# Kernel tuning notes

Hardware: AMD Instinct MI355X
Metric: run time of the kernel (lower is better)

## Reference

```python
import jax, jax.numpy as jnp
import numpy as np

BETA = 1.0
DEPTH = 10
LEVELS = DEPTH - 1          # decision levels along any root->leaf path
NUM_LEAVES = 2 ** LEVELS    # 512
NUM_INTERNAL = NUM_LEAVES - 1  # 511, heap-ordered: root=0, children 2i+1/2i+2


def _tree_paths():
    """For each leaf, the heap indices of its ancestors and the branch taken (0=left,1=right)."""
    anc = np.zeros((NUM_LEAVES, LEVELS), dtype=np.int32)
    bits = np.zeros((NUM_LEAVES, LEVELS), dtype=np.int32)
    for j in range(NUM_LEAVES):
        node = 0
        for t in range(LEVELS):
            bit = (j >> (LEVELS - 1 - t)) & 1
            anc[j, t] = node
            bits[j, t] = bit
            node = 2 * node + 1 + bit
    return jnp.asarray(anc), jnp.asarray(bits)

_ANC, _BITS = _tree_paths()


def setup_inputs() -> dict:
    key = jax.random.key(0)
    k1, k2, k3, k4 = jax.random.split(key, 4)
    B, F, K = 8192, 4096, 1000
    return {
        "xs": jax.random.normal(k1, (B, F), dtype=jnp.float32),
        "W": jax.random.normal(k2, (NUM_INTERNAL, F), dtype=jnp.float32) * (1.0 / np.sqrt(F)),
        "b": jax.random.normal(k3, (NUM_INTERNAL,), dtype=jnp.float32) * 0.01,
        "leaf_params": jax.random.normal(k4, (NUM_LEAVES, K), dtype=jnp.float32),
    }


def reference(xs, W, b, leaf_params):
    # All node projections as one GEMM: [B, NUM_INTERNAL]
    ps = jax.nn.sigmoid(BETA * (xs @ W.T + b))
    # Gather per-leaf ancestor probs: [B, NUM_LEAVES, LEVELS]
    g = ps[:, _ANC]
    edge = jnp.where(_BITS[None] == 1, g, 1.0 - g)
    leaf_prob = jnp.prod(edge, axis=-1)          # [B, NUM_LEAVES]
    dists = jax.nn.softmax(leaf_params, axis=-1)  # [NUM_LEAVES, K]
    return leaf_prob @ dists                      # [B, K]
```

## Files before the change

### kernel.cpp

```cpp
#include <hip/hip_runtime.h>


typedef __bf16 bf16x8 __attribute__((ext_vector_type(8)));
typedef float f32x4 __attribute__((ext_vector_type(4)));
typedef _Float16 f16x8 __attribute__((ext_vector_type(8)));

#define B_DIM 8192
#define F_DIM 4096
#define NI 511
#define NL 512
#define K_DIM 1000
#define KPAD 1024
#define SPLIT 4
#define KCHUNK 1024

#define W_BLKS  1024
#define SM_BLKS 512

__device__ inline unsigned short f2bf(float f) {
    unsigned int u = __float_as_uint(f);
    return (unsigned short)((u + 0x7FFFu + ((u >> 16) & 1u)) >> 16);
}
__device__ inline unsigned int pk_bf16(float a, float b) {
    return (unsigned int)f2bf(a) | ((unsigned int)f2bf(b) << 16);
}
__device__ inline unsigned int pk2_hu(float a, float b) {
    unsigned int ua = __float_as_uint(a) + 0x8000u;
    unsigned int ub = __float_as_uint(b) + 0x8000u;
    return __builtin_amdgcn_perm(ub, ua, 0x07060302u);
}

typedef __attribute__((address_space(1))) const unsigned int guint;
typedef __attribute__((address_space(3))) unsigned int luint;
__device__ inline void gload16(const unsigned short* g, unsigned short* l) {
    __builtin_amdgcn_global_load_lds((guint*)g, (luint*)l, 16, 0, 0);
}

__device__ inline bf16x8 ldb(const unsigned short* Lbase, int r, int kb) {
    const int g = (kb >> 3) ^ (r & 7);
    return *(const bf16x8*)&Lbase[r * 64 + g * 8];
}

__device__ inline float waveMax(float v) {
#pragma unroll
    for (int off = 32; off; off >>= 1) v = fmaxf(v, __shfl_down(v, off, 64));
    return v;
}
__device__ inline float waveSum(float v) {
#pragma unroll
    for (int off = 32; off; off >>= 1) v += __shfl_down(v, off, 64);
    return v;
}

__global__ __launch_bounds__(256) void prep_kernel(
    const float* __restrict__ W, unsigned short* __restrict__ Wb,
    const float* __restrict__ lp, unsigned short* __restrict__ dT)
{
    __shared__ float sred[8];
    const int bid = blockIdx.x;
    const int tid = threadIdx.x;

    if (bid < W_BLKS) {
        const size_t i = ((size_t)bid * 256 + tid) * 8;
        const int row = (int)(i >> 12);
        uint4 h = {0u, 0u, 0u, 0u};
        if (row < NI) {
            const float4 a = *(const float4*)(W + i);
            const float4 b = *(const float4*)(W + i + 4);
            h.x = pk_bf16(a.x, a.y);
            h.y = pk_bf16(a.z, a.w);
            h.z = pk_bf16(b.x, b.y);
            h.w = pk_bf16(b.z, b.w);
        }
        *(uint4*)(Wb + i) = h;
        return;
    }
    const int k = bid - W_BLKS;
    const int lane = tid & 63;
    const int wave = tid >> 6;
    const float* rowp = lp + (size_t)k * K_DIM;

    float vals[4];
    float mx = -3.0e38f;
#pragma unroll
    for (int c = 0; c < 4; ++c) {
        const int n = tid + c * 256;
        vals[c] = (n < K_DIM) ? rowp[n] : -3.0e38f;
        mx = fmaxf(mx, vals[c]);
    }
    mx = waveMax(mx);
    if (lane == 0) sred[wave] = mx;
    __syncthreads();
    const float gmax = fmaxf(fmaxf(sred[0], sred[1]), fmaxf(sred[2], sred[3]));

    float sum = 0.f;
#pragma unroll
    for (int c = 0; c < 4; ++c) {
        const int n = tid + c * 256;
        const float e = (n < K_DIM) ? __expf(vals[c] - gmax) : 0.f;
        vals[c] = e;
        sum += e;
    }
    sum = waveSum(sum);
    if (lane == 0) sred[4 + wave] = sum;
    __syncthreads();
    const float inv = 1.0f / (sred[4] + sred[5] + sred[6] + sred[7]);
#pragma unroll
    for (int c = 0; c < 4; ++c) {
        const int n = tid + c * 256;
        if (n < K_DIM) dT[(size_t)n * NL + k] = f2bf(vals[c] * inv);
    }
}

__global__ __launch_bounds__(256) void gemm1_kernel(
    const float* __restrict__ A, const unsigned short* __restrict__ Bb,
    _Float16* __restrict__ part)
{
    __shared__ __align__(16) unsigned short Al[128 * 64];
    __shared__ __align__(16) unsigned short Bl[2][128 * 64];

    const int id = blockIdx.x;
    const int xcd = id & 7;
    const int jj = (id >> 3) & 15;
    const int mhi = id >> 7;
    const int z = jj >> 2;
    const int nt = jj & 3;
    const int m0 = (mhi * 8 + xcd) * 128;
    const int n0 = nt * 128;
    const int kbeg = z * KCHUNK;

    const int tid = threadIdx.x;
    const int lane = tid & 63;
    const int wave = tid >> 6;
    const int wm = (wave >> 1) * 64;
    const int wn = (wave & 1) * 64;
    const int quad = lane >> 4;
    const int l16 = lane & 15;

    const int rowA = wave * 4 + (lane >> 4);
    const int q = lane & 15;
    const float* gA = A + (size_t)(m0 + rowA) * F_DIM + kbeg + q * 4;

    const int drb = lane >> 3;
    const int cb = ((lane & 7) ^ drb) * 8;
    const unsigned short* gB = Bb + (size_t)(n0 + wave * 8 + drb) * F_DIM + kbeg + cb;
    const int lBoff = wave * 8 * 64;

    const f32x4 zero = {0.f, 0.f, 0.f, 0.f};
    f32x4 acc[4][4];
#pragma unroll
    for (int i = 0; i < 4; ++i)
#pragma unroll
        for (int j2 = 0; j2 < 4; ++j2) acc[i][j2] = zero;

#pragma unroll
    for (int p = 0; p < 4; ++p)
        gload16(gB + (size_t)p * 32 * F_DIM, &Bl[0][lBoff + p * 2048]);
    f32x4 ab[2][8];
#pragma unroll
    for (int p = 0; p < 8; ++p)
        ab[0][p] = *(const f32x4*)(gA + (size_t)p * 16 * F_DIM);

#pragma unroll
    for (int t = 0; t < 16; ++t) {
#pragma unroll
        for (int p = 0; p < 8; ++p) {
            const int r = rowA + p * 16;
            uint2 w;
            w.x = pk2_hu(ab[t & 1][p].x, ab[t & 1][p].y);
            w.y = pk2_hu(ab[t & 1][p].z, ab[t & 1][p].w);
            *(uint2*)&Al[r * 64 + (((q >> 1) ^ (r & 7)) * 8) + (q & 1) * 4] = w;
        }
        __syncthreads();

        if (t < 15) {
#pragma unroll
            for (int p = 0; p < 8; ++p)
                ab[(t + 1) & 1][p] =
                    *(const f32x4*)(gA + (size_t)(t + 1) * 64 + (size_t)p * 16 * F_DIM);
#pragma unroll
            for (int p = 0; p < 4; ++p)
                gload16(gB + (size_t)(t + 1) * 64 + (size_t)p * 32 * F_DIM,
                        &Bl[(t + 1) & 1][lBoff + p * 2048]);
        }

#pragma unroll
        for (int kk = 0; kk < 64; kk += 32) {
            const int kb = kk + quad * 8;
            bf16x8 av[4], bv[4];
#pragma unroll
            for (int i = 0; i < 4; ++i)
                av[i] = ldb(Al, wm + i * 16 + l16, kb);
#pragma unroll
            for (int j2 = 0; j2 < 4; ++j2)
                bv[j2] = ldb(&Bl[t & 1][0], wn + j2 * 16 + l16, kb);
#pragma unroll
            for (int i = 0; i < 4; ++i)
#pragma unroll
                for (int j2 = 0; j2 < 4; ++j2)
                    acc[i][j2] = __builtin_amdgcn_mfma_f32_16x16x32_bf16(av[i], bv[j2], acc[i][j2], 0, 0, 0);
        }
        __syncthreads();
    }

    _Float16* dst = part + (size_t)z * ((size_t)B_DIM * NL);
#pragma unroll
    for (int i = 0; i < 4; ++i) {
        const int mbase = m0 + wm + i * 16 + quad * 4;
#pragma unroll
        for (int j2 = 0; j2 < 4; ++j2) {
            const int n = n0 + wn + j2 * 16 + l16;
#pragma unroll
            for (int r = 0; r < 4; ++r)
                dst[(size_t)(mbase + r) * NL + n] = (_Float16)acc[i][j2][r];
        }
    }
}

__global__ __launch_bounds__(256) void reduce_tree_kernel(
    const _Float16* __restrict__ part, const float* __restrict__ bvec,
    unsigned short* __restrict__ leafbf)
{
    __shared__ float bsh[NL];
    __shared__ float prow[4][NL];

    const int tid = threadIdx.x;
    bsh[tid] = (tid < NI) ? bvec[tid] : 0.0f;
    const int t2 = tid + 256;
    bsh[t2] = (t2 < NI) ? bvec[t2] : 0.0f;

    const int wave = tid >> 6;
    const int lane = tid & 63;
    const int row = blockIdx.x * 4 + wave;
    const size_t base = (size_t)row * NL + lane * 8;

    float v[8] = {0.f, 0.f, 0.f, 0.f, 0.f, 0.f, 0.f, 0.f};
#pragma unroll
    for (int s = 0; s < SPLIT; ++s) {
        const f16x8 h = *(const f16x8*)(part + (size_t)s * ((size_t)B_DIM * NL) + base);
#pragma unroll
        for (int e = 0; e < 8; ++e) v[e] += (float)h[e];
    }
    __syncthreads();

#pragma unroll
    for (int i = 0; i < 8; ++i) {
        const float x = v[i] + bsh[lane * 8 + i];
        prow[wave][lane * 8 + i] = 1.0f / (1.0f + __expf(-x));
    }
    __syncthreads();

    const float* pr = prow[wave];
    float pre = 1.0f;
    int pnode = 0;
#pragma unroll
    for (int t = 5; t >= 0; --t) {
        const int bit = (lane >> t) & 1;
        const float p = pr[pnode];
        pre *= bit ? p : (1.0f - p);
        pnode = 2 * pnode + 1 + bit;
    }
    unsigned short outs[8];
#pragma unroll
    for (int jj = 0; jj < 8; ++jj) {
        float prob = pre;
        int node = pnode;
#pragma unroll
        for (int t = 2; t >= 0; --t) {
            const int bit = (jj >> t) & 1;
            const float p = pr[node];
            prob *= bit ? p : (1.0f - p);
            node = 2 * node + 1 + bit;
        }
        outs[jj] = f2bf(prob);
    }
    uint4 r;
    r.x = (unsigned int)outs[0] | ((unsigned int)outs[1] << 16);
    r.y = (unsigned int)outs[2] | ((unsigned int)outs[3] << 16);
    r.z = (unsigned int)outs[4] | ((unsigned int)outs[5] << 16);
    r.w = (unsigned int)outs[6] | ((unsigned int)outs[7] << 16);
    *(uint4*)(leafbf + (size_t)row * NL + lane * 8) = r;
}

__global__ __launch_bounds__(256) void gemm2_kernel(
    const unsigned short* __restrict__ A, const unsigned short* __restrict__ Bm,
    float* __restrict__ out)
{
    __shared__ __align__(16) unsigned short Al[128 * 64];
    __shared__ __align__(16) unsigned short Bl[128 * 64];

    const int id = blockIdx.x;
    const int xcd = id & 7;
    const int j = id >> 3;
    const int nt = j & 7;
    const int mhi = j >> 3;
    const int m0 = (mhi * 8 + xcd) * 128;
    const int n0 = nt * 128;

    const int tid = threadIdx.x;
    const int lane = tid & 63;
    const int wave = tid >> 6;
    const int wm = (wave >> 1) * 64;
    const int wn = (wave & 1) * 64;
    const int quad = lane >> 4;
    const int l16 = lane & 15;

    const int drb = lane >> 3;
    const int cb = ((lane & 7) ^ drb) * 8;
    const unsigned short* gA = A + (size_t)(m0 + wave * 8 + drb) * NL + cb;
    const unsigned short* gB = Bm + (size_t)(n0 + wave * 8 + drb) * NL + cb;
    unsigned short* lA = &Al[wave * 8 * 64];
    unsigned short* lB = &Bl[wave * 8 * 64];

    const f32x4 zero = {0.f, 0.f, 0.f, 0.f};
    f32x4 acc[4][4];
#pragma unroll
    for (int i = 0; i < 4; ++i)
#pragma unroll
        for (int j2 = 0; j2 < 4; ++j2) acc[i][j2] = zero;

    for (int k0 = 0; k0 < NL; k0 += 64) {
#pragma unroll
        for (int p = 0; p < 4; ++p) {
            gload16(gA + k0 + (size_t)p * 32 * NL, lA + p * 2048);
            gload16(gB + k0 + (size_t)p * 32 * NL, lB + p * 2048);
        }
        __syncthreads();
#pragma unroll
        for (int kk = 0; kk < 64; kk += 32) {
            const int kb = kk + quad * 8;
            bf16x8 av[4], bv[4];
#pragma unroll
            for (int i = 0; i < 4; ++i)
                av[i] = ldb(Al, wm + i * 16 + l16, kb);
#pragma unroll
            for (int j2 = 0; j2 < 4; ++j2)
                bv[j2] = ldb(Bl, wn + j2 * 16 + l16, kb);
#pragma unroll
            for (int i = 0; i < 4; ++i)
#pragma unroll
                for (int j2 = 0; j2 < 4; ++j2)
                    acc[i][j2] = __builtin_amdgcn_mfma_f32_16x16x32_bf16(av[i], bv[j2], acc[i][j2], 0, 0, 0);
        }
        __syncthreads();
    }

#pragma unroll
    for (int i = 0; i < 4; ++i) {
        const int mbase = m0 + wm + i * 16 + quad * 4;
#pragma unroll
        for (int j2 = 0; j2 < 4; ++j2) {
            const int n = n0 + wn + j2 * 16 + l16;
            if (n < K_DIM) {
#pragma unroll
                for (int r = 0; r < 4; ++r)
                    out[(size_t)(mbase + r) * K_DIM + n] = acc[i][j2][r];
            }
        }
    }
}

extern "C" void kernel_launch(void* const* d_in, const int* in_sizes, int n_in,
                              void* d_out, int out_size, void* d_ws, size_t ws_size,
                              hipStream_t stream) {
    const float* xs = (const float*)d_in[0];
    const float* W  = (const float*)d_in[1];
    const float* b  = (const float*)d_in[2];
    const float* lp = (const float*)d_in[3];
    float* out = (float*)d_out;

    const size_t partB = (size_t)B_DIM * NL * 2;
    const size_t leafB = (size_t)B_DIM * NL * 2;
    const size_t dTB   = (size_t)KPAD * NL * 2;

    char* ws = (char*)d_ws;
    _Float16* part = (_Float16*)ws;
    unsigned short* leafbf = (unsigned short*)(ws + SPLIT * partB);
    unsigned short* dT = (unsigned short*)(ws + SPLIT * partB + leafB);
    unsigned short* Wb = (unsigned short*)(ws + SPLIT * partB + leafB + dTB);
    (void)ws_size;

    hipLaunchKernelGGL(prep_kernel, dim3(W_BLKS + SM_BLKS), dim3(256), 0, stream,
                       W, Wb, lp, dT);
    hipLaunchKernelGGL(gemm1_kernel, dim3(8 * 8 * 4 * 4), dim3(256), 0, stream,
                       xs, Wb, part);
    hipLaunchKernelGGL(reduce_tree_kernel, dim3(B_DIM / 4), dim3(256), 0, stream,
                       part, b, leafbf);
    hipLaunchKernelGGL(gemm2_kernel, dim3(8 * 8 * 8), dim3(256), 0, stream,
                       leafbf, dT, out);
}
```

Measured before the change: 287.7 us.

## Halve split-K in gemm1 and deepen its load pipeline with explicit waitcnt barriers

The first GEMM's split-K factor drops from 4 to 2, so each block covers a K chunk of 2048 across 32 iterations. That halves the fp16 partial buffers that must be written and later reduced. The main loop now prefetches two stages ahead, using four B buffers in LDS and two register stages for A. It syncs with manual s_waitcnt and s_barrier plus sched_barrier fences, and launch bounds request 2 blocks per CU. The grid shrinks to 512 blocks, which lowers parallelism per block and raises LDS use per block to about 80KB.

```diff
diff --git a/kernel.cpp b/kernel.cpp
--- a/kernel.cpp
+++ b/kernel.cpp
@@ -11,8 +11,9 @@
 #define NL 512
 #define K_DIM 1000
 #define KPAD 1024
-#define SPLIT 4
-#define KCHUNK 1024
+#define SPLIT 2
+#define KCHUNK 2048
+#define NT_G1 32
 
 #define W_BLKS  1024
 #define SM_BLKS 512
@@ -112,19 +113,19 @@
     }
 }
 
-__global__ __launch_bounds__(256) void gemm1_kernel(
+__global__ __launch_bounds__(256, 2) void gemm1_kernel(
     const float* __restrict__ A, const unsigned short* __restrict__ Bb,
     _Float16* __restrict__ part)
 {
     __shared__ __align__(16) unsigned short Al[128 * 64];
-    __shared__ __align__(16) unsigned short Bl[2][128 * 64];
+    __shared__ __align__(16) unsigned short Bl[4][128 * 64];
 
     const int id = blockIdx.x;
     const int xcd = id & 7;
-    const int jj = (id >> 3) & 15;
-    const int mhi = id >> 7;
-    const int z = jj >> 2;
-    const int nt = jj & 3;
+    const int j = id >> 3;
+    const int nt = j & 3;
+    const int z = (j >> 2) & 1;
+    const int mhi = j >> 3;
     const int m0 = (mhi * 8 + xcd) * 128;
     const int n0 = nt * 128;
     const int kbeg = z * KCHUNK;
@@ -153,55 +154,68 @@
 #pragma unroll
         for (int j2 = 0; j2 < 4; ++j2) acc[i][j2] = zero;
 
+    f32x4 ab[2][8];
 #pragma unroll
     for (int p = 0; p < 4; ++p)
         gload16(gB + (size_t)p * 32 * F_DIM, &Bl[0][lBoff + p * 2048]);
-    f32x4 ab[2][8];
+#pragma unroll
+    for (int p = 0; p < 4; ++p)
+        gload16(gB + 64 + (size_t)p * 32 * F_DIM, &Bl[1][lBoff + p * 2048]);
+    __builtin_amdgcn_sched_barrier(0);
 #pragma unroll
     for (int p = 0; p < 8; ++p)
         ab[0][p] = *(const f32x4*)(gA + (size_t)p * 16 * F_DIM);
-
-#pragma unroll
-    for (int t = 0; t < 16; ++t) {
-#pragma unroll
-        for (int p = 0; p < 8; ++p) {
-            const int r = rowA + p * 16;
-            uint2 w;
-            w.x = pk2_hu(ab[t & 1][p].x, ab[t & 1][p].y);
-            w.y = pk2_hu(ab[t & 1][p].z, ab[t & 1][p].w);
-            *(uint2*)&Al[r * 64 + (((q >> 1) ^ (r & 7)) * 8) + (q & 1) * 4] = w;
-        }
-        __syncthreads();
-
-        if (t < 15) {
-#pragma unroll
-            for (int p = 0; p < 8; ++p)
-                ab[(t + 1) & 1][p] =
-                    *(const f32x4*)(gA + (size_t)(t + 1) * 64 + (size_t)p * 16 * F_DIM);
-#pragma unroll
-            for (int p = 0; p < 4; ++p)
-                gload16(gB + (size_t)(t + 1) * 64 + (size_t)p * 32 * F_DIM,
-                        &Bl[(t + 1) & 1][lBoff + p * 2048]);
-        }
-
-#pragma unroll
-        for (int kk = 0; kk < 64; kk += 32) {
-            const int kb = kk + quad * 8;
-            bf16x8 av[4], bv[4];
-#pragma unroll
-            for (int i = 0; i < 4; ++i)
-                av[i] = ldb(Al, wm + i * 16 + l16, kb);
-#pragma unroll
-            for (int j2 = 0; j2 < 4; ++j2)
-                bv[j2] = ldb(&Bl[t & 1][0], wn + j2 * 16 + l16, kb);
-#pragma unroll
-            for (int i = 0; i < 4; ++i)
-#pragma unroll
-                for (int j2 = 0; j2 < 4; ++j2)
-                    acc[i][j2] = __builtin_amdgcn_mfma_f32_16x16x32_bf16(av[i], bv[j2], acc[i][j2], 0, 0, 0);
-        }
-        __syncthreads();
-    }
+#pragma unroll
+    for (int p = 0; p < 8; ++p)
+        ab[1][p] = *(const f32x4*)(gA + 64 + (size_t)p * 16 * F_DIM);
+    __builtin_amdgcn_sched_barrier(0);
+
+#define G1_ITER(T, DO_ISSUE, WCNT)                                             \
+    {                                                                          \
+        _Pragma("unroll") for (int p = 0; p < 8; ++p) {                        \
+            const int r = rowA + p * 16;                                       \
+            uint2 w;                                                           \
+            w.x = pk2_hu(ab[(T) & 1][p].x, ab[(T) & 1][p].y);                  \
+            w.y = pk2_hu(ab[(T) & 1][p].z, ab[(T) & 1][p].w);                  \
+            *(uint2*)&Al[r * 64 + (((q >> 1) ^ (r & 7)) * 8) + (q & 1) * 4] = w;\
+        }                                                                      \
+        asm volatile("s_waitcnt vmcnt(" #WCNT ") lgkmcnt(0)" ::: "memory");    \
+        __builtin_amdgcn_sched_barrier(0);                                     \
+        __builtin_amdgcn_s_barrier();                                          \
+        __builtin_amdgcn_sched_barrier(0);                                     \
+        if (DO_ISSUE) {                                                        \
+            _Pragma("unroll") for (int p = 0; p < 4; ++p)                      \
+                gload16(gB + (size_t)((T) + 2) * 64 + (size_t)p * 32 * F_DIM,  \
+                        &Bl[((T) + 2) & 3][lBoff + p * 2048]);                 \
+            __builtin_amdgcn_sched_barrier(0);                                 \
+            _Pragma("unroll") for (int p = 0; p < 8; ++p)                      \
+                ab[(T) & 1][p] = *(const f32x4*)(gA + (size_t)((T) + 2) * 64   \
+                                                 + (size_t)p * 16 * F_DIM);    \
+        }                                                                      \
+        _Pragma("unroll") for (int kk = 0; kk < 64; kk += 32) {                \
+            const int kb = kk + quad * 8;                                      \
+            bf16x8 av[4], bv[4];                                               \
+            _Pragma("unroll") for (int i = 0; i < 4; ++i)                      \
+                av[i] = ldb(Al, wm + i * 16 + l16, kb);                        \
+            _Pragma("unroll") for (int j2 = 0; j2 < 4; ++j2)                   \
+                bv[j2] = ldb(&Bl[(T) & 3][0], wn + j2 * 16 + l16, kb);         \
+            _Pragma("unroll") for (int i = 0; i < 4; ++i)                      \
+                _Pragma("unroll") for (int j2 = 0; j2 < 4; ++j2)               \
+                    acc[i][j2] = __builtin_amdgcn_mfma_f32_16x16x32_bf16(      \
+                        av[i], bv[j2], acc[i][j2], 0, 0, 0);                   \
+        }                                                                      \
+        __builtin_amdgcn_sched_barrier(0);                                     \
+        __builtin_amdgcn_s_barrier();                                          \
+        __builtin_amdgcn_sched_barrier(0);                                     \
+    }
+
+#pragma unroll 4
+    for (int t = 0; t < NT_G1 - 4; ++t) G1_ITER(t, 1, 12);
+    G1_ITER(28, 1, 12);
+    G1_ITER(29, 1, 12);
+    G1_ITER(30, 0, 12);
+    G1_ITER(31, 0, 0);
+#undef G1_ITER
 
     _Float16* dst = part + (size_t)z * ((size_t)B_DIM * NL);
 #pragma unroll
@@ -382,7 +396,7 @@
 
     hipLaunchKernelGGL(prep_kernel, dim3(W_BLKS + SM_BLKS), dim3(256), 0, stream,
                        W, Wb, lp, dT);
-    hipLaunchKernelGGL(gemm1_kernel, dim3(8 * 8 * 4 * 4), dim3(256), 0, stream,
+    hipLaunchKernelGGL(gemm1_kernel, dim3(8 * 8 * 2 * 4), dim3(256), 0, stream,
                        xs, Wb, part);
     hipLaunchKernelGGL(reduce_tree_kernel, dim3(B_DIM / 4), dim3(256), 0, stream,
                        part, b, leafbf);
```

After: 263.7 us. 8.4% less time.
